# Performance work log

Measured on AMD Instinct MI355X. Metric: run time of the kernel, lower is better.

Reference implementation:

```python
import jax, jax.numpy as jnp
import numpy as np

PASS = 8        # pass_through_size
FLOW = 16       # flow_size
TRANS = FLOW - PASS  # transform_size = 8
NBINS = 64
HID = 1024


def _conditioner(yA, w1, b1, w2, b2, w3, b3):
    # MLP producing unnormalized positive bin widths Q: [B, TRANS, NBINS]
    h = jax.nn.relu(yA @ w1 + b1)
    h = jax.nn.relu(h @ w2 + b2)
    q = jax.nn.softplus(h @ w3 + b3) + 1e-6  # positivity for slopes
    return q.reshape(-1, TRANS, NBINS)


def setup_inputs() -> dict:
    key = jax.random.key(0)
    ks = jax.random.split(key, 4)
    B = 65536
    y = jax.random.uniform(ks[0], (B, FLOW + 1), dtype=jnp.float32)
    w1 = jax.random.normal(ks[1], (PASS, HID), dtype=jnp.float32) / np.sqrt(PASS)
    w2 = jax.random.normal(ks[2], (HID, HID), dtype=jnp.float32) / np.sqrt(HID)
    w3 = jax.random.normal(ks[3], (HID, TRANS * NBINS), dtype=jnp.float32) / np.sqrt(HID)
    return {
        "y": y,
        "w1": w1, "b1": jnp.zeros((HID,), jnp.float32),
        "w2": w2, "b2": jnp.zeros((HID,), jnp.float32),
        "w3": w3, "b3": jnp.zeros((TRANS * NBINS,), jnp.float32),
    }


def reference(y, w1, b1, w2, b2, w3, b3):
    yA = y[:, :PASS]                      # [B, PASS]
    yB = y[:, PASS:FLOW]                  # [B, TRANS]
    jac = y[:, FLOW:FLOW + 1]             # [B, 1]

    Q = _conditioner(yA, w1, b1, w2, b2, w3, b3)  # [B, TRANS, NBINS]
    Qsum = jnp.cumsum(Q, axis=-1)
    Qnorms = Qsum[:, :, -1:]
    Q = Q / (Qnorms / NBINS)              # slopes per bin
    Qsum = Qsum / Qnorms                  # normalized CDF knots (last == 1)

    # searchsorted(side='left') per row: count of knots strictly below value
    ybins = jnp.sum(Qsum < yB[..., None], axis=-1)          # [B, TRANS] int32
    ybins = jnp.clip(ybins, 0, NBINS - 1)                   # guard fp edge case

    paddedQsum = jnp.pad(Qsum, ((0, 0), (0, 0), (1, 0)))    # prepend 0 knot
    offsets = jnp.take_along_axis(paddedQsum, ybins[..., None], axis=-1)[..., 0]
    slopes = jnp.take_along_axis(Q, ybins[..., None], axis=-1)[..., 0]

    xB = (yB - offsets) / slopes + ybins.astype(jnp.float32) / NBINS
    jac = jac * jnp.prod(1.0 / slopes, axis=-1, keepdims=True)
    return jnp.concatenate((yA, xB, jac), axis=-1)          # [B, FLOW+1]
```

## Files before the change

### kernel.cpp

```cpp
#include <hip/hip_runtime.h>
#include <hip/hip_fp16.h>

#define HID 1024
#define QCOLS 512
#define KP 2048
#define NT 48

typedef _Float16 f16x8 __attribute__((ext_vector_type(8)));
typedef float f32x4 __attribute__((ext_vector_type(4)));

__global__ void tconv_both(const float* __restrict__ w2, __half* __restrict__ w2t,
                           const float* __restrict__ w3, __half* __restrict__ w3t) {
  __shared__ float tile[32][33];
  const int z = blockIdx.z;
  const int N = z ? QCOLS : HID;
  if (blockIdx.x * 32 >= N) return;
  const float* src = z ? w3 : w2;
  __half* dst = z ? w3t : w2t;
  int n0 = blockIdx.x * 32, k0 = blockIdx.y * 32;
  int tx = threadIdx.x, ty = threadIdx.y;
  for (int i = ty; i < 32; i += 8)
    tile[i][tx] = src[(size_t)(k0 + i) * N + n0 + tx];
  __syncthreads();
  for (int i = ty; i < 32; i += 8) {
    float v = tile[tx][i] * 256.f;
    __half h = __float2half(v);
    size_t o = (size_t)(n0 + i) * KP + k0 + tx;
    dst[o] = h;
    dst[o + 1024] = __float2half(v - __half2float(h));
  }
}

__global__ __launch_bounds__(256)
void h1k(const float* __restrict__ y, const float* __restrict__ w1,
         const float* __restrict__ b1, __half* __restrict__ h1,
         int row0, int nrows) {
  const int t = threadIdx.x & 127;
  const int rl = threadIdx.x >> 7;
  const long r = (long)blockIdx.x * 2 + rl;
  if (r >= nrows) return;
  const float* yr = y + (size_t)(row0 + r) * 17;
  float yv[8];
#pragma unroll
  for (int k = 0; k < 8; ++k) yv[k] = yr[k];
  const int c0 = t * 8;
  f32x4 a0 = *(const f32x4*)(b1 + c0);
  f32x4 a1 = *(const f32x4*)(b1 + c0 + 4);
#pragma unroll
  for (int k = 0; k < 8; ++k) {
    const f32x4 w0 = *(const f32x4*)(w1 + k * HID + c0);
    const f32x4 w1v = *(const f32x4*)(w1 + k * HID + c0 + 4);
#pragma unroll
    for (int j = 0; j < 4; ++j) {
      a0[j] = fmaf(yv[k], w0[j], a0[j]);
      a1[j] = fmaf(yv[k], w1v[j], a1[j]);
    }
  }
  f16x8 hi, lo;
#pragma unroll
  for (int j = 0; j < 8; ++j) {
    float v = fmaxf(j < 4 ? a0[j] : a1[j - 4], 0.f) * 64.f;
    _Float16 h = (_Float16)v;
    hi[j] = h;
    lo[j] = (_Float16)(v - (float)h);
  }
  *(f16x8*)(h1 + (size_t)r * KP + c0) = hi;
  *(f16x8*)(h1 + (size_t)r * KP + c0 + 1024) = lo;
}

template <int ACT, int BN>
__device__ __forceinline__
void gemm_ring_body(const __half* __restrict__ A, const __half* __restrict__ Bt,
                    const float* __restrict__ bias, __half* __restrict__ Co,
                    float* __restrict__ Cf, int ldc) {
  constexpr int NFRAG = BN / 64;
  constexpr int BNB = BN * 64;
  constexpr int SLOT = 16384 + BNB;
  constexpr int LPS = 2 + BN / 128;
  __shared__ char lds[4 * SLOT];
  const int tid = threadIdx.x;
  const int lane = tid & 63, wave = tid >> 6;
  const int p = lane & 15, ql = lane >> 4;
  const int wm = wave >> 2, wn = wave & 3;

  const int gx = gridDim.x, nwg = gx * gridDim.y;
  const int bid = blockIdx.y * gx + blockIdx.x;
  const int q8 = nwg >> 3, r8 = nwg & 7;
  const int xcd = bid & 7, lxi = bid >> 3;
  const int swz = (xcd < r8 ? xcd * (q8 + 1) : r8 * (q8 + 1) + (xcd - r8) * q8) + lxi;
  const size_t row_blk = (size_t)(swz / gx) * 256;
  const size_t col_blk = (size_t)(swz % gx) * BN;

  int a_off[8], b_off[NFRAG];
#pragma unroll
  for (int m = 0; m < 8; ++m) {
    int r = wm * 128 + m * 16 + p;
    a_off[m] = r * 64 + ((ql ^ ((r >> 1) & 3)) << 4);
  }
#pragma unroll
  for (int n = 0; n < NFRAG; ++n) {
    int r = wn * (BN / 4) + n * 16 + p;
    b_off[n] = r * 64 + ((ql ^ ((r >> 1) & 3)) << 4);
  }

  const int idx0 = tid, idx1 = tid + 512;
  const int sr0 = idx0 >> 2, sq0 = (idx0 & 3) ^ ((sr0 >> 1) & 3);
  const int sr1 = idx1 >> 2, sq1 = (idx1 & 3) ^ ((sr1 >> 1) & 3);

  auto gload = [&](const __half* g, char* l) {
    __builtin_amdgcn_global_load_lds((__attribute__((address_space(1))) void*)g,
        (__attribute__((address_space(3))) void*)l, 16, 0, 0);
  };

  auto stage = [&](int q) {
    int kt = q >> 1; if (kt > NT - 1) kt = NT - 1;
    const int h = q & 1;
    const int lk = kt * 64;
    const int ak = ((lk >= 2048) ? 1024 : 0) + (lk & 1023) + h * 32;
    const int bk = ((lk >= 1024 && lk < 2048) ? 1024 : 0) + (lk & 1023) + h * 32;
    char* base = lds + (q & 3) * SLOT;
    char* pb = base + 16384;
    gload(A + (row_blk + sr0) * (size_t)KP + ak + sq0 * 8, base + idx0 * 16);
    gload(A + (row_blk + sr1) * (size_t)KP + ak + sq1 * 8, base + idx1 * 16);
    gload(Bt + (col_blk + sr0) * (size_t)KP + bk + sq0 * 8, pb + idx0 * 16);
    if constexpr (BN == 256)
      gload(Bt + (col_blk + sr1) * (size_t)KP + bk + sq1 * 8, pb + idx1 * 16);
  };

  auto wait_ring = [&]() {
    if constexpr (LPS == 4) asm volatile("s_waitcnt vmcnt(8)" ::: "memory");
    else                    asm volatile("s_waitcnt vmcnt(6)" ::: "memory");
  };

  stage(0); stage(1); stage(2);
  wait_ring();
  __builtin_amdgcn_s_barrier();

  f32x4 acc[8][NFRAG] = {};

  for (int ph = 0; ph < NT * 2; ++ph) {
    const char* base = lds + (ph & 3) * SLOT;
    const char* pB = base + 16384;
    f16x8 af[8], bfr[NFRAG];
#pragma unroll
    for (int m = 0; m < 8; ++m) af[m] = *(const f16x8*)(base + a_off[m]);
#pragma unroll
    for (int n = 0; n < NFRAG; ++n) bfr[n] = *(const f16x8*)(pB + b_off[n]);
    stage(ph + 3);
    __builtin_amdgcn_sched_barrier(0);
    __builtin_amdgcn_s_barrier();
    __builtin_amdgcn_sched_barrier(0);
    __builtin_amdgcn_s_setprio(1);
#pragma unroll
    for (int m = 0; m < 8; ++m)
#pragma unroll
      for (int n = 0; n < NFRAG; ++n)
        acc[m][n] = __builtin_amdgcn_mfma_f32_16x16x32_f16(af[m], bfr[n], acc[m][n], 0, 0, 0);
    __builtin_amdgcn_s_setprio(0);
    wait_ring();
    __builtin_amdgcn_sched_barrier(0);
    __builtin_amdgcn_s_barrier();
    __builtin_amdgcn_sched_barrier(0);
  }

  const float unscale = 1.f / 16384.f;
#pragma unroll
  for (int n = 0; n < NFRAG; ++n) {
    const size_t col = col_blk + wn * (BN / 4) + n * 16 + p;
    const float bv = bias[col];
#pragma unroll
    for (int m = 0; m < 8; ++m) {
      const size_t row0 = row_blk + wm * 128 + m * 16 + ql * 4;
#pragma unroll
      for (int j = 0; j < 4; ++j) {
        float v = acc[m][n][j] * unscale + bv;
        const size_t o = (row0 + j) * (size_t)ldc + col;
        if constexpr (ACT == 0) {
          float r = fmaxf(v, 0.f) * 64.f;
          __half hh = __float2half(r);
          Co[o] = hh;
          Co[o + 1024] = __float2half(r - __half2float(hh));
        } else {
          float sp = fmaxf(v, 0.f) + log1pf(expf(-fabsf(v)));
          Cf[o] = sp + 1e-6f;
        }
      }
    }
  }
}

__global__ __launch_bounds__(512, 2)
void g2relu(const __half* __restrict__ A, const __half* __restrict__ B,
            const float* __restrict__ bias, __half* __restrict__ Co) {
  gemm_ring_body<0, 256>(A, B, bias, Co, nullptr, KP);
}

__global__ __launch_bounds__(512, 2)
void g3soft(const __half* __restrict__ A, const __half* __restrict__ B,
            const float* __restrict__ bias, float* __restrict__ Cf) {
  gemm_ring_body<1, 128>(A, B, bias, nullptr, Cf, QCOLS);
}

__global__ __launch_bounds__(256)
void pwl_epi(const float* __restrict__ y, const float* __restrict__ q,
             float* __restrict__ out, int row0, int nrows) {
  const int wave = threadIdx.x >> 6, lane = threadIdx.x & 63;
  const int r = blockIdx.x * 4 + wave;
  if (r >= nrows) return;
  const float* yr = y + (size_t)(row0 + r) * 17;
  float* orow = out + (size_t)(row0 + r) * 17;
  const float* qr = q + (size_t)r * QCOLS;
  float prod_inv = 1.f;
#pragma unroll
  for (int t = 0; t < 8; ++t) {
    const float qv = qr[t * 64 + lane];
    float s = qv;
#pragma unroll
    for (int d = 1; d < 64; d <<= 1) {
      float u = __shfl_up(s, d);
      if (lane >= d) s += u;
    }
    const float total = __shfl(s, 63);
    const float sn = s / total;
    const float dnorm = total * 0.015625f;
    const float slope_l = qv / dnorm;
    const float yb = yr[8 + t];
    const unsigned long long m = __ballot(sn < yb);
    int bin = (int)__popcll(m);
    bin = bin > 63 ? 63 : bin;
    const float off_g = __shfl(sn, bin > 0 ? bin - 1 : 0);
    const float off = (bin == 0) ? 0.f : off_g;
    const float sl = __shfl(slope_l, bin);
    const float xB = (yb - off) / sl + (float)bin * 0.015625f;
    if (lane == t) orow[8 + t] = xB;
    prod_inv *= (1.f / sl);
  }
  if (lane < 8) orow[lane] = yr[lane];
  if (lane == 8) orow[16] = yr[16] * prod_inv;
}

extern "C" void kernel_launch(void* const* d_in, const int* in_sizes, int n_in,
                              void* d_out, int out_size, void* d_ws, size_t ws_size,
                              hipStream_t stream) {
  const float* y  = (const float*)d_in[0];
  const float* w1 = (const float*)d_in[1];
  const float* b1 = (const float*)d_in[2];
  const float* w2 = (const float*)d_in[3];
  const float* b2 = (const float*)d_in[4];
  const float* w3 = (const float*)d_in[5];
  const float* b3 = (const float*)d_in[6];
  float* out = (float*)d_out;
  const long Btot = in_sizes[0] / 17;

  char* ws = (char*)d_ws;
  __half* w2t = (__half*)ws;
  __half* w3t = (__half*)(ws + (4u << 20));
  const size_t fixed = (size_t)6 << 20;

  const size_t avail = ws_size > fixed ? ws_size - fixed : 0;
  long maxrows = (long)(avail / 8192);
  long chunk = 256;
  for (long c = 65536; c >= 256; c >>= 1) {
    if (c <= maxrows && c <= Btot) { chunk = c; break; }
  }

  __half* h1buf = (__half*)(ws + fixed);
  __half* h2buf = (__half*)(ws + fixed + (size_t)chunk * 4096);
  float* qbuf = (float*)h1buf;

  tconv_both<<<dim3(32, 32, 2), dim3(32, 8), 0, stream>>>(w2, w2t, w3, w3t);

  for (long row0 = 0; row0 < Btot; row0 += chunk) {
    const int nr = (int)((Btot - row0 < chunk) ? (Btot - row0) : chunk);
    h1k<<<(nr + 1) / 2, 256, 0, stream>>>(y, w1, b1, h1buf, (int)row0, nr);
    g2relu<<<dim3(HID / 256, nr / 256), 512, 0, stream>>>(h1buf, w2t, b2, h2buf);
    g3soft<<<dim3(QCOLS / 128, nr / 256), 512, 0, stream>>>(h2buf, w3t, b3, qbuf);
    pwl_epi<<<(nr + 3) / 4, 256, 0, stream>>>(y, qbuf, out, (int)row0, nr);
  }
}
```

Before: 913.4 us.

## Use 256x128 tiles with 3-slot LDS ring and higher occupancy for both GEMMs

Drops the BN=256 template variant so the hidden-layer GEMM also uses 256x128 tiles, doubling its grid in the column dimension. The LDS ring shrinks from four slots to three, with prefetch depth two instead of three, and launch bounds go from 2 to 4 workgroups per CU. The aim is more resident waves to hide latency and smaller LDS and register use. In exchange, A-tile reuse per workgroup drops and the shallower prefetch gives less slack against global-load latency.

```diff
diff --git a/kernel.cpp b/kernel.cpp
--- a/kernel.cpp
+++ b/kernel.cpp
@@ -68,16 +68,13 @@
   *(f16x8*)(h1 + (size_t)r * KP + c0 + 1024) = lo;
 }
 
-template <int ACT, int BN>
+template <int ACT>
 __device__ __forceinline__
 void gemm_ring_body(const __half* __restrict__ A, const __half* __restrict__ Bt,
                     const float* __restrict__ bias, __half* __restrict__ Co,
                     float* __restrict__ Cf, int ldc) {
-  constexpr int NFRAG = BN / 64;
-  constexpr int BNB = BN * 64;
-  constexpr int SLOT = 16384 + BNB;
-  constexpr int LPS = 2 + BN / 128;
-  __shared__ char lds[4 * SLOT];
+  constexpr int SLOT = 16384 + 8192;
+  __shared__ char lds[3 * SLOT];
   const int tid = threadIdx.x;
   const int lane = tid & 63, wave = tid >> 6;
   const int p = lane & 15, ql = lane >> 4;
@@ -89,17 +86,17 @@
   const int xcd = bid & 7, lxi = bid >> 3;
   const int swz = (xcd < r8 ? xcd * (q8 + 1) : r8 * (q8 + 1) + (xcd - r8) * q8) + lxi;
   const size_t row_blk = (size_t)(swz / gx) * 256;
-  const size_t col_blk = (size_t)(swz % gx) * BN;
-
-  int a_off[8], b_off[NFRAG];
+  const size_t col_blk = (size_t)(swz % gx) * 128;
+
+  int a_off[8], b_off[2];
 #pragma unroll
   for (int m = 0; m < 8; ++m) {
     int r = wm * 128 + m * 16 + p;
     a_off[m] = r * 64 + ((ql ^ ((r >> 1) & 3)) << 4);
   }
 #pragma unroll
-  for (int n = 0; n < NFRAG; ++n) {
-    int r = wn * (BN / 4) + n * 16 + p;
+  for (int n = 0; n < 2; ++n) {
+    int r = wn * 32 + n * 16 + p;
     b_off[n] = r * 64 + ((ql ^ ((r >> 1) & 3)) << 4);
   }
 
@@ -112,41 +109,37 @@
         (__attribute__((address_space(3))) void*)l, 16, 0, 0);
   };
 
-  auto stage = [&](int q) {
+  auto stage = [&](int q, int slot) {
     int kt = q >> 1; if (kt > NT - 1) kt = NT - 1;
     const int h = q & 1;
     const int lk = kt * 64;
     const int ak = ((lk >= 2048) ? 1024 : 0) + (lk & 1023) + h * 32;
     const int bk = ((lk >= 1024 && lk < 2048) ? 1024 : 0) + (lk & 1023) + h * 32;
-    char* base = lds + (q & 3) * SLOT;
+    char* base = lds + slot * SLOT;
     char* pb = base + 16384;
     gload(A + (row_blk + sr0) * (size_t)KP + ak + sq0 * 8, base + idx0 * 16);
     gload(A + (row_blk + sr1) * (size_t)KP + ak + sq1 * 8, base + idx1 * 16);
     gload(Bt + (col_blk + sr0) * (size_t)KP + bk + sq0 * 8, pb + idx0 * 16);
-    if constexpr (BN == 256)
-      gload(Bt + (col_blk + sr1) * (size_t)KP + bk + sq1 * 8, pb + idx1 * 16);
   };
 
-  auto wait_ring = [&]() {
-    if constexpr (LPS == 4) asm volatile("s_waitcnt vmcnt(8)" ::: "memory");
-    else                    asm volatile("s_waitcnt vmcnt(6)" ::: "memory");
-  };
-
-  stage(0); stage(1); stage(2);
-  wait_ring();
+  stage(0, 0);
+  stage(1, 1);
+  asm volatile("s_waitcnt vmcnt(3)" ::: "memory");
   __builtin_amdgcn_s_barrier();
 
-  f32x4 acc[8][NFRAG] = {};
-
+  f32x4 acc[8][2] = {};
+
+  int cur = 0;
   for (int ph = 0; ph < NT * 2; ++ph) {
-    const char* base = lds + (ph & 3) * SLOT;
+    const char* base = lds + cur * SLOT;
     const char* pB = base + 16384;
-    f16x8 af[8], bfr[NFRAG];
+    f16x8 af[8], bfr[2];
 #pragma unroll
     for (int m = 0; m < 8; ++m) af[m] = *(const f16x8*)(base + a_off[m]);
 #pragma unroll
-    for (int n = 0; n < NFRAG; ++n) bfr[n] = *(const f16x8*)(pB + b_off[n]);
-    stage(ph + 3);
+    for (int n = 0; n < 2; ++n) bfr[n] = *(const f16x8*)(pB + b_off[n]);
+    const int nslot = cur == 0 ? 2 : cur - 1;
+    stage(ph + 2, nslot);
     __builtin_amdgcn_sched_barrier(0);
     __builtin_amdgcn_s_barrier();
     __builtin_amdgcn_sched_barrier(0);
@@ -154,19 +147,20 @@
 #pragma unroll
     for (int m = 0; m < 8; ++m)
 #pragma unroll
-      for (int n = 0; n < NFRAG; ++n)
+      for (int n = 0; n < 2; ++n)
         acc[m][n] = __builtin_amdgcn_mfma_f32_16x16x32_f16(af[m], bfr[n], acc[m][n], 0, 0, 0);
     __builtin_amdgcn_s_setprio(0);
-    wait_ring();
+    asm volatile("s_waitcnt vmcnt(3)" ::: "memory");
     __builtin_amdgcn_sched_barrier(0);
     __builtin_amdgcn_s_barrier();
     __builtin_amdgcn_sched_barrier(0);
+    cur = cur == 2 ? 0 : cur + 1;
   }
 
   const float unscale = 1.f / 16384.f;
 #pragma unroll
-  for (int n = 0; n < NFRAG; ++n) {
-    const size_t col = col_blk + wn * (BN / 4) + n * 16 + p;
+  for (int n = 0; n < 2; ++n) {
+    const size_t col = col_blk + wn * 32 + n * 16 + p;
     const float bv = bias[col];
 #pragma unroll
     for (int m = 0; m < 8; ++m) {
@@ -189,16 +183,16 @@
   }
 }
 
-__global__ __launch_bounds__(512, 2)
+__global__ __launch_bounds__(512, 4)
 void g2relu(const __half* __restrict__ A, const __half* __restrict__ B,
             const float* __restrict__ bias, __half* __restrict__ Co) {
-  gemm_ring_body<0, 256>(A, B, bias, Co, nullptr, KP);
-}
-
-__global__ __launch_bounds__(512, 2)
+  gemm_ring_body<0>(A, B, bias, Co, nullptr, KP);
+}
+
+__global__ __launch_bounds__(512, 4)
 void g3soft(const __half* __restrict__ A, const __half* __restrict__ B,
             const float* __restrict__ bias, float* __restrict__ Cf) {
-  gemm_ring_body<1, 128>(A, B, bias, nullptr, Cf, QCOLS);
+  gemm_ring_body<1>(A, B, bias, nullptr, Cf, QCOLS);
 }
 
 __global__ __launch_bounds__(256)
@@ -273,7 +267,7 @@
   for (long row0 = 0; row0 < Btot; row0 += chunk) {
     const int nr = (int)((Btot - row0 < chunk) ? (Btot - row0) : chunk);
     h1k<<<(nr + 1) / 2, 256, 0, stream>>>(y, w1, b1, h1buf, (int)row0, nr);
-    g2relu<<<dim3(HID / 256, nr / 256), 512, 0, stream>>>(h1buf, w2t, b2, h2buf);
+    g2relu<<<dim3(HID / 128, nr / 256), 512, 0, stream>>>(h1buf, w2t, b2, h2buf);
     g3soft<<<dim3(QCOLS / 128, nr / 256), 512, 0, stream>>>(h2buf, w3t, b3, qbuf);
     pwl_epi<<<(nr + 3) / 4, 256, 0, stream>>>(y, qbuf, out, (int)row0, nr);
   }
```

After: 917.5 us. No clear change (+0.4%).
